# Performance work log

Measured on AMD Instinct MI355X. Metric: run time of the kernel, lower is better.

The kernel has to match this reference:

```python
import jax, jax.numpy as jnp
import numpy as np

HEAD_SIZE = 128  # matches init head_size; original scales by global head_size**-0.5


def setup_inputs() -> dict:
    key = jax.random.key(0)
    k1, k2, k3, k4 = jax.random.split(key, 4)
    B, T, C, D = 16, 2048, 1024, HEAD_SIZE
    x = jax.random.normal(k1, (B, T, C), dtype=jnp.float32)
    # torch Linear weight is [out,in]; store transposed so forward is x @ W
    Wq = jax.random.normal(k2, (C, D), dtype=jnp.float32) * (C ** -0.5)
    Wk = jax.random.normal(k3, (C, D), dtype=jnp.float32) * (C ** -0.5)
    Wv = jax.random.normal(k4, (C, D), dtype=jnp.float32) * (C ** -0.5)
    return {"x": x, "Wq": Wq, "Wk": Wk, "Wv": Wv}


def reference(x, Wq, Wk, Wv):
    # x: [B,T,C]; projections -> [B,T,D]
    q = x @ Wq
    k = x @ Wk
    v = x @ Wv
    T = x.shape[1]
    scale = HEAD_SIZE ** -0.5
    # scores: [B,T,T]
    wei = jnp.einsum("btd,bsd->bts", q, k) * scale
    causal = jnp.tril(jnp.ones((T, T), dtype=bool))  # tril buffer
    wei = jnp.where(causal, wei, -jnp.inf)
    wei = jax.nn.softmax(wei, axis=-1)
    # dropout is identity in eval mode (deterministic reference)
    return wei @ v  # [B,T,D]
```

## Files before the change

### kernel.cpp

```cpp
#include <hip/hip_runtime.h>
#include <hip/hip_bf16.h>

typedef short bf16x8 __attribute__((ext_vector_type(8)));
typedef float f32x4 __attribute__((ext_vector_type(4)));
typedef unsigned short u16x4 __attribute__((ext_vector_type(4)));

#define B_ 16
#define T_ 2048
#define C_ 1024
#define D_ 128
#define M_ (B_ * T_)

static __device__ __forceinline__ unsigned short f2bf(float f) {
    unsigned int u = __builtin_bit_cast(unsigned int, f);
    unsigned int r = (u + 0x7fffu + ((u >> 16) & 1u)) >> 16;
    return (unsigned short)r;
}

__global__ void wt_kernel(const float* __restrict__ Wq, const float* __restrict__ Wk,
                          const float* __restrict__ Wv, unsigned short* __restrict__ Wt) {
    int idx = blockIdx.x * 256 + threadIdx.x;
    int o   = idx >> 17;
    int rem = idx & 131071;
    int k   = rem >> 7;
    int n   = rem & 127;
    const float* W = (o == 0) ? Wq : (o == 1) ? Wk : Wv;
    Wt[o * (D_ * C_) + n * C_ + k] = f2bf(W[rem]);
}

#define ASTR 68
#define BSTR 68

__launch_bounds__(512, 1)
__global__ void qkv_kernel(const float* __restrict__ x, const unsigned short* __restrict__ Wt,
                           unsigned short* __restrict__ Q, unsigned short* __restrict__ K,
                           unsigned short* __restrict__ Vt) {
    __shared__ unsigned short Alds[2][128 * ASTR];
    __shared__ unsigned short Blds[2][384 * BSTR];

    const int tid  = threadIdx.x;
    const int lane = tid & 63;
    const int w    = tid >> 6;
    const int wr   = w >> 2;
    const int wc   = w & 3;
    const int lr   = lane & 15;
    const int lk   = lane >> 4;
    const int m0   = blockIdx.x * 128;

    const int axr = tid >> 4;
    const int axc = (tid & 15) * 4;
    const int bxr = tid >> 3;
    const int bxc = (tid & 7) * 8;

    float4 ar[4];
    bf16x8 br[6];

    auto stage_load = [&](int k0) {
#pragma unroll
        for (int j = 0; j < 4; ++j)
            ar[j] = *(const float4*)(x + (size_t)(m0 + axr + j * 32) * C_ + k0 + axc);
#pragma unroll
        for (int j = 0; j < 6; ++j)
            br[j] = *(const bf16x8*)(Wt + (size_t)(bxr + j * 64) * C_ + k0 + bxc);
    };
    auto stage_write = [&](int buf) {
#pragma unroll
        for (int j = 0; j < 4; ++j) {
            u16x4 v;
            v[0] = f2bf(ar[j].x); v[1] = f2bf(ar[j].y);
            v[2] = f2bf(ar[j].z); v[3] = f2bf(ar[j].w);
            *(u16x4*)&Alds[buf][(axr + j * 32) * ASTR + axc] = v;
        }
#pragma unroll
        for (int j = 0; j < 6; ++j)
            *(bf16x8*)&Blds[buf][(bxr + j * 64) * BSTR + bxc] = br[j];
    };

    f32x4 acc[4][6] = {};

    auto compute = [&](int buf) {
#pragma unroll
        for (int kk = 0; kk < 2; ++kk) {
            bf16x8 a[4], b[6];
#pragma unroll
            for (int rb = 0; rb < 4; ++rb)
                a[rb] = *(bf16x8*)&Alds[buf][(wr * 64 + rb * 16 + lr) * ASTR + kk * 32 + lk * 8];
#pragma unroll
            for (int nb = 0; nb < 6; ++nb)
                b[nb] = *(bf16x8*)&Blds[buf][(wc * 96 + nb * 16 + lr) * BSTR + kk * 32 + lk * 8];
#pragma unroll
            for (int rb = 0; rb < 4; ++rb)
#pragma unroll
                for (int nb = 0; nb < 6; ++nb)
                    acc[rb][nb] = __builtin_amdgcn_mfma_f32_16x16x32_bf16(a[rb], b[nb], acc[rb][nb], 0, 0, 0);
        }
    };

    stage_load(0);
    stage_write(0);
    for (int t = 0; t < 16; ++t) {
        __syncthreads();
        if (t < 15) stage_load((t + 1) * 64);
        compute(t & 1);
        if (t < 15) stage_write((t + 1) & 1);
    }

    const float qscale = 0.08838834764831845f;
    const int b  = m0 / T_;
    const int t0 = m0 % T_;
#pragma unroll
    for (int rb = 0; rb < 4; ++rb) {
#pragma unroll
        for (int nb = 0; nb < 6; ++nb) {
            const int row0 = wr * 64 + rb * 16 + lk * 4;
            const int col  = wc * 96 + nb * 16 + lr;
            const int o    = col >> 7;
            const int d    = col & 127;
            f32x4 a = acc[rb][nb];
            if (o == 0) {
#pragma unroll
                for (int r = 0; r < 4; ++r)
                    Q[(size_t)(m0 + row0 + r) * D_ + d] = f2bf(a[r] * qscale);
            } else if (o == 1) {
#pragma unroll
                for (int r = 0; r < 4; ++r)
                    K[(size_t)(m0 + row0 + r) * D_ + d] = f2bf(a[r]);
            } else {
                u16x4 pv;
#pragma unroll
                for (int r = 0; r < 4; ++r) pv[r] = f2bf(a[r]);
                *(u16x4*)&Vt[((size_t)b * D_ + d) * T_ + t0 + row0] = pv;
            }
        }
    }
}

#define KSTR 132
#define VSTR 68
#define PSTR 68

__launch_bounds__(256, 2)
__global__ void attn_kernel(const unsigned short* __restrict__ Q, const unsigned short* __restrict__ K,
                            const unsigned short* __restrict__ Vt, float* __restrict__ out) {
    __shared__ unsigned short Klds[2][64 * KSTR];
    __shared__ unsigned short Vlds[2][128 * VSTR];
    __shared__ unsigned short Plds[4][16 * PSTR];

    const int tid  = threadIdx.x;
    const int lane = tid & 63;
    const int w    = tid >> 6;
    const int lr   = lane & 15;
    const int lk   = lane >> 4;

    const int batch = blockIdx.x >> 4;
    const int pair  = blockIdx.x & 15;

    const unsigned short* Qb = Q  + (size_t)batch * T_ * D_;
    const unsigned short* Kb = K  + (size_t)batch * T_ * D_;
    const unsigned short* Vb = Vt + (size_t)batch * D_ * T_;
    float* outb = out + (size_t)batch * T_ * D_;

    const int kxr = tid >> 4;
    const int kxc = (tid & 15) * 8;
    const int vxr = tid >> 3;
    const int vxc = (tid & 7) * 8;

    bf16x8 kr[4], vr[4];
    auto kv_load = [&](int kvt) {
        const int kv0 = kvt * 64;
#pragma unroll
        for (int j = 0; j < 4; ++j)
            kr[j] = *(const bf16x8*)(Kb + (size_t)(kv0 + kxr + j * 16) * D_ + kxc);
#pragma unroll
        for (int j = 0; j < 4; ++j)
            vr[j] = *(const bf16x8*)(Vb + (size_t)(vxr + j * 32) * T_ + kv0 + vxc);
    };
    auto kv_write = [&](int buf) {
#pragma unroll
        for (int j = 0; j < 4; ++j)
            *(bf16x8*)&Klds[buf][(kxr + j * 16) * KSTR + kxc] = kr[j];
#pragma unroll
        for (int j = 0; j < 4; ++j)
            *(bf16x8*)&Vlds[buf][(vxr + j * 32) * VSTR + vxc] = vr[j];
    };

    for (int half = 0; half < 2; ++half) {
        const int qt = (half == 0) ? pair : (31 - pair);
        const int qw = qt * 64 + w * 16;

        bf16x8 qf[4];
#pragma unroll
        for (int c = 0; c < 4; ++c)
            qf[c] = *(const bf16x8*)(Qb + (size_t)(qw + lr) * D_ + lk * 8 + c * 32);

        f32x4 o_acc[8] = {};
        float mrun[4] = {-1e30f, -1e30f, -1e30f, -1e30f};
        float lrun[4] = {0.f, 0.f, 0.f, 0.f};

        __syncthreads();
        kv_load(0);
        kv_write(0);

        for (int kvt = 0; kvt <= qt; ++kvt) {
            const int cur = kvt & 1;
            __syncthreads();
            if (kvt < qt) kv_load(kvt + 1);

            f32x4 s[4];
#pragma unroll
            for (int nb = 0; nb < 4; ++nb) {
                f32x4 a = {};
#pragma unroll
                for (int c = 0; c < 4; ++c) {
                    bf16x8 kf = *(bf16x8*)&Klds[cur][(nb * 16 + lr) * KSTR + lk * 8 + c * 32];
                    a = __builtin_amdgcn_mfma_f32_16x16x32_bf16(qf[c], kf, a, 0, 0, 0);
                }
                s[nb] = a;
            }

            if (kvt == qt) {
#pragma unroll
                for (int nb = 0; nb < 4; ++nb)
#pragma unroll
                    for (int r = 0; r < 4; ++r) {
                        int qg = qw + lk * 4 + r;
                        int kg = kvt * 64 + nb * 16 + lr;
                        if (kg > qg) s[nb][r] = -1e30f;
                    }
            }

            float scale_[4];
#pragma unroll
            for (int r = 0; r < 4; ++r) {
                float mx = fmaxf(fmaxf(s[0][r], s[1][r]), fmaxf(s[2][r], s[3][r]));
                mx = fmaxf(mx, __shfl_xor(mx, 1));
                mx = fmaxf(mx, __shfl_xor(mx, 2));
                mx = fmaxf(mx, __shfl_xor(mx, 4));
                mx = fmaxf(mx, __shfl_xor(mx, 8));
                float mnew = fmaxf(mrun[r], mx);
                scale_[r]  = __expf(mrun[r] - mnew);
                mrun[r]    = mnew;
                lrun[r]   *= scale_[r];
            }
#pragma unroll
            for (int db = 0; db < 8; ++db)
#pragma unroll
                for (int r = 0; r < 4; ++r) o_acc[db][r] *= scale_[r];

#pragma unroll
            for (int nb = 0; nb < 4; ++nb)
#pragma unroll
                for (int r = 0; r < 4; ++r) {
                    float p = __expf(s[nb][r] - mrun[r]);
                    lrun[r] += p;
                    Plds[w][(lk * 4 + r) * PSTR + nb * 16 + lr] = f2bf(p);
                }
            asm volatile("s_waitcnt lgkmcnt(0)" ::: "memory");
            __builtin_amdgcn_sched_barrier(0);

            bf16x8 pa[2];
#pragma unroll
            for (int c = 0; c < 2; ++c)
                pa[c] = *(bf16x8*)&Plds[w][lr * PSTR + lk * 8 + c * 32];
#pragma unroll
            for (int db = 0; db < 8; ++db) {
                f32x4 oo = o_acc[db];
#pragma unroll
                for (int c = 0; c < 2; ++c) {
                    bf16x8 vf = *(bf16x8*)&Vlds[cur][(db * 16 + lr) * VSTR + lk * 8 + c * 32];
                    oo = __builtin_amdgcn_mfma_f32_16x16x32_bf16(pa[c], vf, oo, 0, 0, 0);
                }
                o_acc[db] = oo;
            }

            if (kvt < qt) kv_write(cur ^ 1);
        }

#pragma unroll
        for (int r = 0; r < 4; ++r) {
            float sgm = lrun[r];
            sgm += __shfl_xor(sgm, 1);
            sgm += __shfl_xor(sgm, 2);
            sgm += __shfl_xor(sgm, 4);
            sgm += __shfl_xor(sgm, 8);
            lrun[r] = 1.0f / sgm;
        }
#pragma unroll
        for (int db = 0; db < 8; ++db)
#pragma unroll
            for (int r = 0; r < 4; ++r)
                outb[(size_t)(qw + lk * 4 + r) * D_ + db * 16 + lr] = o_acc[db][r] * lrun[r];
    }
}

extern "C" void kernel_launch(void* const* d_in, const int* in_sizes, int n_in,
                              void* d_out, int out_size, void* d_ws, size_t ws_size,
                              hipStream_t stream) {
    const float* x  = (const float*)d_in[0];
    const float* Wq = (const float*)d_in[1];
    const float* Wk = (const float*)d_in[2];
    const float* Wv = (const float*)d_in[3];

    unsigned short* Wt  = (unsigned short*)d_ws;
    unsigned short* Qw  = (unsigned short*)((char*)d_ws + (1 << 20));
    unsigned short* Kw  = Qw + (size_t)M_ * D_;
    unsigned short* Vtw = Kw + (size_t)M_ * D_;

    hipLaunchKernelGGL(wt_kernel, dim3(1536), dim3(256), 0, stream, Wq, Wk, Wv, Wt);
    hipLaunchKernelGGL(qkv_kernel, dim3(256), dim3(512), 0, stream, x, Wt, Qw, Kw, Vtw);
    hipLaunchKernelGGL(attn_kernel, dim3(256), dim3(256), 0, stream, Qw, Kw, Vtw, (float*)d_out);
}
```

Before: 101.4 us.

## Halve GEMM tiles and split attention pair blocks into separate blocks

The QKV projection GEMM now uses 64-row tiles with a K-step of 32, so it launches 512 blocks with higher occupancy hints instead of 256 single-occupancy blocks. The attention kernel no longer has each block process a paired short and long query tile in sequence. Each query tile gets its own block (512 blocks), with the long tiles scheduled after the short ones. The aim is to fill the 256 CUs better and add latency hiding, at the cost of less data reuse per block and possible load imbalance in attention.

New measurement: 104.7 us. +3.2%, slower.

```diff
diff --git a/kernel.cpp b/kernel.cpp
--- a/kernel.cpp
+++ b/kernel.cpp
@@ -28,14 +28,14 @@
     Wt[o * (D_ * C_) + n * C_ + k] = f2bf(W[rem]);
 }
 
-#define ASTR 68
-#define BSTR 68
-
-__launch_bounds__(512, 1)
+#define ASTR 36
+#define BSTR 36
+
+__launch_bounds__(512, 4)
 __global__ void qkv_kernel(const float* __restrict__ x, const unsigned short* __restrict__ Wt,
                            unsigned short* __restrict__ Q, unsigned short* __restrict__ K,
                            unsigned short* __restrict__ Vt) {
-    __shared__ unsigned short Alds[2][128 * ASTR];
+    __shared__ unsigned short Alds[2][64 * ASTR];
     __shared__ unsigned short Blds[2][384 * BSTR];
 
     const int tid  = threadIdx.x;
@@ -45,74 +45,65 @@
     const int wc   = w & 3;
     const int lr   = lane & 15;
     const int lk   = lane >> 4;
-    const int m0   = blockIdx.x * 128;
-
-    const int axr = tid >> 4;
-    const int axc = (tid & 15) * 4;
-    const int bxr = tid >> 3;
-    const int bxc = (tid & 7) * 8;
-
-    float4 ar[4];
-    bf16x8 br[6];
+    const int m0   = blockIdx.x * 64;
+
+    const int axr = tid >> 3;
+    const int axc = (tid & 7) * 4;
+    const int bxr = tid >> 2;
+    const int bxc = (tid & 3) * 8;
+
+    float4 ar;
+    bf16x8 br[3];
 
     auto stage_load = [&](int k0) {
-#pragma unroll
-        for (int j = 0; j < 4; ++j)
-            ar[j] = *(const float4*)(x + (size_t)(m0 + axr + j * 32) * C_ + k0 + axc);
-#pragma unroll
-        for (int j = 0; j < 6; ++j)
-            br[j] = *(const bf16x8*)(Wt + (size_t)(bxr + j * 64) * C_ + k0 + bxc);
+        ar = *(const float4*)(x + (size_t)(m0 + axr) * C_ + k0 + axc);
+#pragma unroll
+        for (int j = 0; j < 3; ++j)
+            br[j] = *(const bf16x8*)(Wt + (size_t)(bxr + j * 128) * C_ + k0 + bxc);
     };
     auto stage_write = [&](int buf) {
-#pragma unroll
-        for (int j = 0; j < 4; ++j) {
-            u16x4 v;
-            v[0] = f2bf(ar[j].x); v[1] = f2bf(ar[j].y);
-            v[2] = f2bf(ar[j].z); v[3] = f2bf(ar[j].w);
-            *(u16x4*)&Alds[buf][(axr + j * 32) * ASTR + axc] = v;
-        }
-#pragma unroll
-        for (int j = 0; j < 6; ++j)
-            *(bf16x8*)&Blds[buf][(bxr + j * 64) * BSTR + bxc] = br[j];
-    };
-
-    f32x4 acc[4][6] = {};
+        u16x4 v;
+        v[0] = f2bf(ar.x); v[1] = f2bf(ar.y); v[2] = f2bf(ar.z); v[3] = f2bf(ar.w);
+        *(u16x4*)&Alds[buf][axr * ASTR + axc] = v;
+#pragma unroll
+        for (int j = 0; j < 3; ++j)
+            *(bf16x8*)&Blds[buf][(bxr + j * 128) * BSTR + bxc] = br[j];
+    };
+
+    f32x4 acc[2][6] = {};
 
     auto compute = [&](int buf) {
-#pragma unroll
-        for (int kk = 0; kk < 2; ++kk) {
-            bf16x8 a[4], b[6];
-#pragma unroll
-            for (int rb = 0; rb < 4; ++rb)
-                a[rb] = *(bf16x8*)&Alds[buf][(wr * 64 + rb * 16 + lr) * ASTR + kk * 32 + lk * 8];
+        bf16x8 a[2], b[6];
+#pragma unroll
+        for (int rb = 0; rb < 2; ++rb)
+            a[rb] = *(bf16x8*)&Alds[buf][(wr * 32 + rb * 16 + lr) * ASTR + lk * 8];
+#pragma unroll
+        for (int nb = 0; nb < 6; ++nb)
+            b[nb] = *(bf16x8*)&Blds[buf][(wc * 96 + nb * 16 + lr) * BSTR + lk * 8];
+#pragma unroll
+        for (int rb = 0; rb < 2; ++rb)
 #pragma unroll
             for (int nb = 0; nb < 6; ++nb)
-                b[nb] = *(bf16x8*)&Blds[buf][(wc * 96 + nb * 16 + lr) * BSTR + kk * 32 + lk * 8];
-#pragma unroll
-            for (int rb = 0; rb < 4; ++rb)
-#pragma unroll
-                for (int nb = 0; nb < 6; ++nb)
-                    acc[rb][nb] = __builtin_amdgcn_mfma_f32_16x16x32_bf16(a[rb], b[nb], acc[rb][nb], 0, 0, 0);
-        }
+                acc[rb][nb] = __builtin_amdgcn_mfma_f32_16x16x32_bf16(a[rb], b[nb], acc[rb][nb], 0, 0, 0);
     };
 
     stage_load(0);
     stage_write(0);
-    for (int t = 0; t < 16; ++t) {
+    for (int t = 0; t < 32; ++t) {
         __syncthreads();
-        if (t < 15) stage_load((t + 1) * 64);
+        if (t < 31) stage_load((t + 1) * 32);
         compute(t & 1);
-        if (t < 15) stage_write((t + 1) & 1);
+        if (t < 31) stage_write((t + 1) & 1);
     }
 
     const float qscale = 0.08838834764831845f;
     const int b  = m0 / T_;
     const int t0 = m0 % T_;
 #pragma unroll
-    for (int rb = 0; rb < 4; ++rb) {
+    for (int rb = 0; rb < 2; ++rb) {
 #pragma unroll
         for (int nb = 0; nb < 6; ++nb) {
-            const int row0 = wr * 64 + rb * 16 + lk * 4;
+            const int row0 = wr * 32 + rb * 16 + lk * 4;
             const int col  = wc * 96 + nb * 16 + lr;
             const int o    = col >> 7;
             const int d    = col & 127;
@@ -152,8 +143,10 @@
     const int lr   = lane & 15;
     const int lk   = lane >> 4;
 
-    const int batch = blockIdx.x >> 4;
-    const int pair  = blockIdx.x & 15;
+    int bid = blockIdx.x;
+    int batch, qt;
+    if (bid < 256) { batch = bid >> 4; qt = bid & 15; }
+    else           { bid -= 256; batch = bid >> 4; qt = 31 - (bid & 15); }
 
     const unsigned short* Qb = Q  + (size_t)batch * T_ * D_;
     const unsigned short* Kb = K  + (size_t)batch * T_ * D_;
@@ -184,113 +177,109 @@
             *(bf16x8*)&Vlds[buf][(vxr + j * 32) * VSTR + vxc] = vr[j];
     };
 
-    for (int half = 0; half < 2; ++half) {
-        const int qt = (half == 0) ? pair : (31 - pair);
-        const int qw = qt * 64 + w * 16;
-
-        bf16x8 qf[4];
-#pragma unroll
-        for (int c = 0; c < 4; ++c)
-            qf[c] = *(const bf16x8*)(Qb + (size_t)(qw + lr) * D_ + lk * 8 + c * 32);
-
-        f32x4 o_acc[8] = {};
-        float mrun[4] = {-1e30f, -1e30f, -1e30f, -1e30f};
-        float lrun[4] = {0.f, 0.f, 0.f, 0.f};
-
+    const int qw = qt * 64 + w * 16;
+
+    bf16x8 qf[4];
+#pragma unroll
+    for (int c = 0; c < 4; ++c)
+        qf[c] = *(const bf16x8*)(Qb + (size_t)(qw + lr) * D_ + lk * 8 + c * 32);
+
+    f32x4 o_acc[8] = {};
+    float mrun[4] = {-1e30f, -1e30f, -1e30f, -1e30f};
+    float lrun[4] = {0.f, 0.f, 0.f, 0.f};
+
+    kv_load(0);
+    kv_write(0);
+
+    for (int kvt = 0; kvt <= qt; ++kvt) {
+        const int cur = kvt & 1;
         __syncthreads();
-        kv_load(0);
-        kv_write(0);
-
-        for (int kvt = 0; kvt <= qt; ++kvt) {
-            const int cur = kvt & 1;
-            __syncthreads();
-            if (kvt < qt) kv_load(kvt + 1);
-
-            f32x4 s[4];
-#pragma unroll
-            for (int nb = 0; nb < 4; ++nb) {
-                f32x4 a = {};
-#pragma unroll
-                for (int c = 0; c < 4; ++c) {
-                    bf16x8 kf = *(bf16x8*)&Klds[cur][(nb * 16 + lr) * KSTR + lk * 8 + c * 32];
-                    a = __builtin_amdgcn_mfma_f32_16x16x32_bf16(qf[c], kf, a, 0, 0, 0);
+        if (kvt < qt) kv_load(kvt + 1);
+
+        f32x4 s[4];
+#pragma unroll
+        for (int nb = 0; nb < 4; ++nb) {
+            f32x4 a = {};
+#pragma unroll
+            for (int c = 0; c < 4; ++c) {
+                bf16x8 kf = *(bf16x8*)&Klds[cur][(nb * 16 + lr) * KSTR + lk * 8 + c * 32];
+                a = __builtin_amdgcn_mfma_f32_16x16x32_bf16(qf[c], kf, a, 0, 0, 0);
+            }
+            s[nb] = a;
+        }
+
+        if (kvt == qt) {
+#pragma unroll
+            for (int nb = 0; nb < 4; ++nb)
+#pragma unroll
+                for (int r = 0; r < 4; ++r) {
+                    int qg = qw + lk * 4 + r;
+                    int kg = kvt * 64 + nb * 16 + lr;
+                    if (kg > qg) s[nb][r] = -1e30f;
                 }
-                s[nb] = a;
+        }
+
+        float scale_[4];
+#pragma unroll
+        for (int r = 0; r < 4; ++r) {
+            float mx = fmaxf(fmaxf(s[0][r], s[1][r]), fmaxf(s[2][r], s[3][r]));
+            mx = fmaxf(mx, __shfl_xor(mx, 1));
+            mx = fmaxf(mx, __shfl_xor(mx, 2));
+            mx = fmaxf(mx, __shfl_xor(mx, 4));
+            mx = fmaxf(mx, __shfl_xor(mx, 8));
+            float mnew = fmaxf(mrun[r], mx);
+            scale_[r]  = __expf(mrun[r] - mnew);
+            mrun[r]    = mnew;
+            lrun[r]   *= scale_[r];
+        }
+#pragma unroll
+        for (int db = 0; db < 8; ++db)
+#pragma unroll
+            for (int r = 0; r < 4; ++r) o_acc[db][r] *= scale_[r];
+
+#pragma unroll
+        for (int nb = 0; nb < 4; ++nb)
+#pragma unroll
+            for (int r = 0; r < 4; ++r) {
+                float p = __expf(s[nb][r] - mrun[r]);
+                lrun[r] += p;
+                Plds[w][(lk * 4 + r) * PSTR + nb * 16 + lr] = f2bf(p);
             }
-
-            if (kvt == qt) {
-#pragma unroll
-                for (int nb = 0; nb < 4; ++nb)
-#pragma unroll
-                    for (int r = 0; r < 4; ++r) {
-                        int qg = qw + lk * 4 + r;
-                        int kg = kvt * 64 + nb * 16 + lr;
-                        if (kg > qg) s[nb][r] = -1e30f;
-                    }
+        asm volatile("s_waitcnt lgkmcnt(0)" ::: "memory");
+        __builtin_amdgcn_sched_barrier(0);
+
+        bf16x8 pa[2];
+#pragma unroll
+        for (int c = 0; c < 2; ++c)
+            pa[c] = *(bf16x8*)&Plds[w][lr * PSTR + lk * 8 + c * 32];
+#pragma unroll
+        for (int db = 0; db < 8; ++db) {
+            f32x4 oo = o_acc[db];
+#pragma unroll
+            for (int c = 0; c < 2; ++c) {
+                bf16x8 vf = *(bf16x8*)&Vlds[cur][(db * 16 + lr) * VSTR + lk * 8 + c * 32];
+                oo = __builtin_amdgcn_mfma_f32_16x16x32_bf16(pa[c], vf, oo, 0, 0, 0);
             }
-
-            float scale_[4];
-#pragma unroll
-            for (int r = 0; r < 4; ++r) {
-                float mx = fmaxf(fmaxf(s[0][r], s[1][r]), fmaxf(s[2][r], s[3][r]));
-                mx = fmaxf(mx, __shfl_xor(mx, 1));
-                mx = fmaxf(mx, __shfl_xor(mx, 2));
-                mx = fmaxf(mx, __shfl_xor(mx, 4));
-                mx = fmaxf(mx, __shfl_xor(mx, 8));
-                float mnew = fmaxf(mrun[r], mx);
-                scale_[r]  = __expf(mrun[r] - mnew);
-                mrun[r]    = mnew;
-                lrun[r]   *= scale_[r];
-            }
-#pragma unroll
-            for (int db = 0; db < 8; ++db)
-#pragma unroll
-                for (int r = 0; r < 4; ++r) o_acc[db][r] *= scale_[r];
-
-#pragma unroll
-            for (int nb = 0; nb < 4; ++nb)
-#pragma unroll
-                for (int r = 0; r < 4; ++r) {
-                    float p = __expf(s[nb][r] - mrun[r]);
-                    lrun[r] += p;
-                    Plds[w][(lk * 4 + r) * PSTR + nb * 16 + lr] = f2bf(p);
-                }
-            asm volatile("s_waitcnt lgkmcnt(0)" ::: "memory");
-            __builtin_amdgcn_sched_barrier(0);
-
-            bf16x8 pa[2];
-#pragma unroll
-            for (int c = 0; c < 2; ++c)
-                pa[c] = *(bf16x8*)&Plds[w][lr * PSTR + lk * 8 + c * 32];
-#pragma unroll
-            for (int db = 0; db < 8; ++db) {
-                f32x4 oo = o_acc[db];
-#pragma unroll
-                for (int c = 0; c < 2; ++c) {
-                    bf16x8 vf = *(bf16x8*)&Vlds[cur][(db * 16 + lr) * VSTR + lk * 8 + c * 32];
-                    oo = __builtin_amdgcn_mfma_f32_16x16x32_bf16(pa[c], vf, oo, 0, 0, 0);
-                }
-                o_acc[db] = oo;
-            }
-
-            if (kvt < qt) kv_write(cur ^ 1);
-        }
-
-#pragma unroll
-        for (int r = 0; r < 4; ++r) {
-            float sgm = lrun[r];
-            sgm += __shfl_xor(sgm, 1);
-            sgm += __shfl_xor(sgm, 2);
-            sgm += __shfl_xor(sgm, 4);
-            sgm += __shfl_xor(sgm, 8);
-            lrun[r] = 1.0f / sgm;
-        }
-#pragma unroll
-        for (int db = 0; db < 8; ++db)
-#pragma unroll
-            for (int r = 0; r < 4; ++r)
-                outb[(size_t)(qw + lk * 4 + r) * D_ + db * 16 + lr] = o_acc[db][r] * lrun[r];
+            o_acc[db] = oo;
+        }
+
+        if (kvt < qt) kv_write(cur ^ 1);
     }
+
+#pragma unroll
+    for (int r = 0; r < 4; ++r) {
+        float sgm = lrun[r];
+        sgm += __shfl_xor(sgm, 1);
+        sgm += __shfl_xor(sgm, 2);
+        sgm += __shfl_xor(sgm, 4);
+        sgm += __shfl_xor(sgm, 8);
+        lrun[r] = 1.0f / sgm;
+    }
+#pragma unroll
+    for (int db = 0; db < 8; ++db)
+#pragma unroll
+        for (int r = 0; r < 4; ++r)
+            outb[(size_t)(qw + lk * 4 + r) * D_ + db * 16 + lr] = o_acc[db][r] * lrun[r];
 }
 
 extern "C" void kernel_launch(void* const* d_in, const int* in_sizes, int n_in,
@@ -307,6 +296,6 @@
     unsigned short* Vtw = Kw + (size_t)M_ * D_;
 
     hipLaunchKernelGGL(wt_kernel, dim3(1536), dim3(256), 0, stream, Wq, Wk, Wv, Wt);
-    hipLaunchKernelGGL(qkv_kernel, dim3(256), dim3(512), 0, stream, x, Wt, Qw, Kw, Vtw);
-    hipLaunchKernelGGL(attn_kernel, dim3(256), dim3(256), 0, stream, Qw, Kw, Vtw, (float*)d_out);
-}
+    hipLaunchKernelGGL(qkv_kernel, dim3(512), dim3(512), 0, stream, x, Wt, Qw, Kw, Vtw);
+    hipLaunchKernelGGL(attn_kernel, dim3(512), dim3(256), 0, stream, Qw, Kw, Vtw, (float*)d_out);
+}
```
